# Kernel tuning notes

Measured on AMD Instinct MI355X. Metric: run time of the kernel, lower is better.

## Reference

```python
import jax, jax.numpy as jnp
import numpy as np

SEGMENT_LENGTHS = [1024, 2048, 4096]
DILATION_RATES = [1, 2, 4]


def setup_inputs() -> dict:
    key = jax.random.key(0)
    kq, kk, kv = jax.random.split(key, 3)
    shape = (2, 4096, 12, 64)  # [batch, seq_len, num_heads, head_dim]
    return {
        "query": jax.random.normal(kq, shape, dtype=jnp.float32),
        "key": jax.random.normal(kk, shape, dtype=jnp.float32),
        "value": jax.random.normal(kv, shape, dtype=jnp.float32),
        "is_causal": 0,
    }


def _group_attention(q, k, v, g, r, offset, is_causal):
    """Dilated segment attention for one head group.

    q/k/v: [b, n, hg, d] (head slice for this group).
    Segments of length g; within each segment attend only at positions
    offset, offset+r, ... (m = g // r tokens). Output scattered back to
    those positions; other positions are zero (LongNet semantics).
    """
    b, n, h, d = q.shape
    s = n // g  # number of segments
    m = g // r  # dilated tokens per segment
    idx = offset + r * jnp.arange(m)
    qs = q.reshape(b, s, g, h, d)[:, :, idx]  # [b, s, m, h, d]
    ks = k.reshape(b, s, g, h, d)[:, :, idx]
    vs = v.reshape(b, s, g, h, d)[:, :, idx]
    scale = 1.0 / jnp.sqrt(jnp.asarray(d, dtype=q.dtype))
    scores = jnp.einsum("bsqhd,bskhd->bshqk", qs, ks) * scale  # [b, s, h, m, m]
    if is_causal:
        mask = jnp.tril(jnp.ones((m, m), dtype=bool))
        scores = jnp.where(mask, scores, jnp.finfo(scores.dtype).min)
    probs = jax.nn.softmax(scores, axis=-1)
    o = jnp.einsum("bshqk,bskhd->bsqhd", probs, vs)  # [b, s, m, h, d]
    out = jnp.zeros((b, s, g, h, d), dtype=q.dtype).at[:, :, idx].set(o)
    return out.reshape(b, n, h, d)


def reference(query, key, value, is_causal):
    # dist not initialized -> sequence-parallel split/gather are identity;
    # forward reduces to ImprovedDilatedAttention on full tensors.
    b, n, h, d = query.shape
    ngroups = len(SEGMENT_LENGTHS)
    hpg = h // ngroups  # heads per group (disjoint head slices)
    causal = bool(is_causal)
    outs = []
    for i, (g, r) in enumerate(zip(SEGMENT_LENGTHS, DILATION_RATES)):
        offset = i % r
        hmin, hmax = i * hpg, (i + 1) * hpg
        outs.append(
            _group_attention(
                query[:, :, hmin:hmax],
                key[:, :, hmin:hmax],
                value[:, :, hmin:hmax],
                g, r, offset, causal,
            )
        )
    return jnp.concatenate(outs, axis=2)  # [b, n, h, d]
```

## Files before the change

kernel.cpp:

```cpp
#include <hip/hip_runtime.h>
#include <hip/hip_bf16.h>

typedef __attribute__((ext_vector_type(8))) short short8;
typedef __attribute__((ext_vector_type(4))) float f32x4;

#define NTILE 16

static __device__ __forceinline__ unsigned pk2(float x, float y) {
  __hip_bfloat162 h = __float22bfloat162_rn(make_float2(x, y));
  unsigned u; __builtin_memcpy(&u, &h, 4); return u;
}

static __device__ __forceinline__ short8 cvt8(float4 a, float4 b) {
  union { unsigned u[4]; short8 s; } r;
  r.u[0] = pk2(a.x, a.y); r.u[1] = pk2(a.z, a.w);
  r.u[2] = pk2(b.x, b.y); r.u[3] = pk2(b.z, b.w);
  return r.s;
}

static __device__ __forceinline__ void gll16(const void* g, void* l) {
  __builtin_amdgcn_global_load_lds(
      (__attribute__((address_space(1))) void*)const_cast<void*>(g),
      (__attribute__((address_space(3))) void*)(l), 16, 0, 0);
}

struct InstInfo { long base0; int stride; };
static __device__ __forceinline__ InstInfo decode_inst(int inst) {
  const int gi    = (inst < 32) ? 0 : ((inst < 48) ? 1 : 2);
  const int local = inst - ((gi == 0) ? 0 : ((gi == 1) ? 32 : 48));
  const int segs  = 4 >> gi;
  const int g     = 1024 << gi;
  const int offs  = gi;
  const int h     = local & 3;
  const int rem   = local >> 2;
  const int seg   = rem & (segs - 1);
  const int b     = rem >> (2 - gi);
  const int hh    = gi * 4 + h;
  InstInfo r;
  r.base0  = ((long)(b * 4096 + seg * g + offs) * 12 + hh) * 64;
  r.stride = (1 << gi) * 768;
  return r;
}

__global__ __launch_bounds__(256)
void pack_kv(const float* __restrict__ Kg, const float* __restrict__ Vg,
             unsigned short* __restrict__ Ks, unsigned short* __restrict__ Vts,
             float* __restrict__ Og)
{
  __shared__ float vtmp[64][65];
  const int tid   = threadIdx.x;
  const int lid   = blockIdx.x;
  const int inst  = lid % 56;
  const int chunk = lid / 56;
  const int gi    = (inst < 32) ? 0 : ((inst < 48) ? 1 : 2);
  InstInfo I = decode_inst(inst);

  {
    const int tok = tid >> 2, part = tid & 3;
    const long ro = I.base0 + (long)(chunk * 64 + tok) * I.stride + part * 16;
    const float4 k0 = *(const float4*)(Kg + ro);
    const float4 k1 = *(const float4*)(Kg + ro + 4);
    const float4 k2 = *(const float4*)(Kg + ro + 8);
    const float4 k3 = *(const float4*)(Kg + ro + 12);
    uint4 ka, kb;
    ka.x = pk2(k0.x,k0.y); ka.y = pk2(k0.z,k0.w); ka.z = pk2(k1.x,k1.y); ka.w = pk2(k1.z,k1.w);
    kb.x = pk2(k2.x,k2.y); kb.y = pk2(k2.z,k2.w); kb.z = pk2(k3.x,k3.y); kb.w = pk2(k3.z,k3.w);
    unsigned short* kd = Ks + ((long)inst*1024 + chunk*64 + tok)*64;
    const int c0 = (2*part)     ^ (tok & 7);
    const int c1 = (2*part + 1) ^ (tok & 7);
    *(uint4*)(kd + c0*8) = ka;
    *(uint4*)(kd + c1*8) = kb;

    const float4 w0 = *(const float4*)(Vg + ro);
    const float4 w1 = *(const float4*)(Vg + ro + 4);
    const float4 w2 = *(const float4*)(Vg + ro + 8);
    const float4 w3 = *(const float4*)(Vg + ro + 12);
    float* c = &vtmp[part*16][0] + tok;
    c[0*65]=w0.x;  c[1*65]=w0.y;  c[2*65]=w0.z;  c[3*65]=w0.w;
    c[4*65]=w1.x;  c[5*65]=w1.y;  c[6*65]=w1.z;  c[7*65]=w1.w;
    c[8*65]=w2.x;  c[9*65]=w2.y;  c[10*65]=w2.z; c[11*65]=w2.w;
    c[12*65]=w3.x; c[13*65]=w3.y; c[14*65]=w3.z; c[15*65]=w3.w;
  }
  __syncthreads();
  {
    const int d = tid >> 2, kp = tid & 3;
    float v[16];
#pragma unroll
    for (int i = 0; i < 16; ++i) v[i] = vtmp[d][kp*16 + i];
    unsigned short* vd = Vts + ((long)inst*64 + d)*1024 + chunk*64;
#pragma unroll
    for (int s = 0; s < 2; ++s) {
      const int pos = (kp*2 + s) ^ (d & 7);
      uint4 w;
      w.x = pk2(v[8*s+0], v[8*s+1]); w.y = pk2(v[8*s+2], v[8*s+3]);
      w.z = pk2(v[8*s+4], v[8*s+5]); w.w = pk2(v[8*s+6], v[8*s+7]);
      *(uint4*)(vd + pos*8) = w;
    }
  }

  const float4 z4 = make_float4(0.f, 0.f, 0.f, 0.f);
  if (gi == 1) {
    for (int i = tid; i < 64*16; i += 256) {
      const int t = i >> 4, pp = i & 15;
      float* op = Og + I.base0 + (long)(chunk*128 + 2*t + 0 - 1) * 768 + pp*4;
      *(float4*)op = z4;
    }
  } else if (gi == 2) {
    for (int i = tid; i < 192*16; i += 256) {
      const int row_i = i >> 4, pp = i & 15;
      const int t = row_i / 3, ddi = row_i - 3*t;
      const int dd = ddi + (ddi >= 2 ? 1 : 0);
      float* op = Og + I.base0 + (long)(chunk*256 + 4*t + dd - 2) * 768 + pp*4;
      *(float4*)op = z4;
    }
  }
}

__global__ __launch_bounds__(256, 4)
void dilated_attn2(const float* __restrict__ Qg,
                   const unsigned short* __restrict__ Ks,
                   const unsigned short* __restrict__ Vts,
                   const int* __restrict__ causal_flag,
                   float* __restrict__ Og)
{
  __shared__ __align__(16) unsigned short K_lds[2][64][64];
  __shared__ __align__(16) unsigned short V_lds[2][64][64];
  __shared__ __align__(16) unsigned short P_lds[4][16][64];

  const int tid  = threadIdx.x;
  const int wave = tid >> 6;
  const int lane = tid & 63;
  const int l15  = lane & 15;
  const int l4   = lane >> 4;
  const int sw   = l15 & 7;

  const int lid  = blockIdx.x;
  const int inst = lid % 56;
  const int qt   = lid / 56;
  InstInfo I = decode_inst(inst);
  const int causal = *causal_flag;

  const float qscale = 0.125f * 1.44269504088896340736f;
  short8 b_q[2][2];
  int qrowf[2];
#pragma unroll
  for (int qf = 0; qf < 2; ++qf) {
    qrowf[qf] = qt*128 + wave*32 + qf*16 + l15;
    const float* qp = Qg + I.base0 + (long)qrowf[qf] * I.stride + l4 * 8;
#pragma unroll
    for (int ks = 0; ks < 2; ++ks) {
      float4 v0 = *(const float4*)(qp + ks*32);
      float4 v1 = *(const float4*)(qp + ks*32 + 4);
      v0.x *= qscale; v0.y *= qscale; v0.z *= qscale; v0.w *= qscale;
      v1.x *= qscale; v1.y *= qscale; v1.z *= qscale; v1.w *= qscale;
      b_q[qf][ks] = cvt8(v0, v1);
    }
  }

  short8 ones8;
  {
    union { unsigned u[4]; short8 s; } r;
    r.u[0] = r.u[1] = r.u[2] = r.u[3] = 0x3F803F80u;
    ones8 = r.s;
  }

  const unsigned short* KsI  = Ks  + (long)inst * (1024*64);
  const unsigned short* VtsI = Vts + (long)inst * (64*1024);
  const int vrow = lane >> 3;
  const int vcol = (lane & 7) * 8;

  f32x4 Oacc[2][4];
  f32x4 accl[2];
#pragma unroll
  for (int qf = 0; qf < 2; ++qf) {
    accl[qf] = (f32x4){0.f,0.f,0.f,0.f};
#pragma unroll
    for (int n = 0; n < 4; ++n) Oacc[qf][n] = (f32x4){0.f,0.f,0.f,0.f};
  }

#define STAGE2(BUF, KT) do {                                                      \
    const long tko = (long)(KT) * 4096;                                           \
    gll16(KsI  + tko + (long)(wave*8     + vrow)*64 + vcol, &K_lds[BUF][wave*8][0]);     \
    gll16(KsI  + tko + (long)((wave+4)*8 + vrow)*64 + vcol, &K_lds[BUF][(wave+4)*8][0]); \
    const long vko = (long)(KT) * 64;                                             \
    gll16(VtsI + (long)(wave*8     + vrow)*1024 + vko + vcol, &V_lds[BUF][wave*8][0]);     \
    gll16(VtsI + (long)((wave+4)*8 + vrow)*1024 + vko + vcol, &V_lds[BUF][(wave+4)*8][0]); \
  } while (0)

  STAGE2(0, 0);
  __syncthreads();

  for (int kt = 0; kt < NTILE; ++kt) {
    const int cur = kt & 1;
    if (kt + 1 < NTILE) STAGE2(cur ^ 1, kt + 1);

    f32x4 S[2][4];
#pragma unroll
    for (int n = 0; n < 4; ++n) {
      short8 kA = *(const short8*)&K_lds[cur][n*16 + l15][((l4 ^ sw) & 7) * 8];
      short8 kB = *(const short8*)&K_lds[cur][n*16 + l15][(((4 + l4) ^ sw) & 7) * 8];
      __builtin_amdgcn_s_setprio(1);
      f32x4 a0 = (f32x4){0.f,0.f,0.f,0.f};
      a0 = __builtin_amdgcn_mfma_f32_16x16x32_bf16(kA, b_q[0][0], a0, 0,0,0);
      a0 = __builtin_amdgcn_mfma_f32_16x16x32_bf16(kB, b_q[0][1], a0, 0,0,0);
      S[0][n] = a0;
      f32x4 a1 = (f32x4){0.f,0.f,0.f,0.f};
      a1 = __builtin_amdgcn_mfma_f32_16x16x32_bf16(kA, b_q[1][0], a1, 0,0,0);
      a1 = __builtin_amdgcn_mfma_f32_16x16x32_bf16(kB, b_q[1][1], a1, 0,0,0);
      S[1][n] = a1;
      __builtin_amdgcn_s_setprio(0);
    }

    if (causal) {
#pragma unroll
      for (int qf = 0; qf < 2; ++qf)
#pragma unroll
        for (int n = 0; n < 4; ++n)
#pragma unroll
          for (int j = 0; j < 4; ++j) {
            int ktok = kt*64 + n*16 + l4*4 + j;
            if (ktok > qrowf[qf]) S[qf][n][j] = -INFINITY;
          }
    }

    short8 ap[2][2];
#pragma unroll
    for (int qf = 0; qf < 2; ++qf) {
      unsigned up[4][2];
#pragma unroll
      for (int n = 0; n < 4; ++n)
#pragma unroll
        for (int s = 0; s < 2; ++s) {
          float p0 = __builtin_amdgcn_exp2f(S[qf][n][2*s]);
          float p1 = __builtin_amdgcn_exp2f(S[qf][n][2*s+1]);
          up[n][s] = pk2(p0, p1);
        }
#pragma unroll
      for (int n = 0; n < 4; ++n) {
        const int colblk = (2*n + (l4 >> 1)) ^ sw;
        *(uint2*)&P_lds[wave][l15][colblk*8 + (l4 & 1)*4] = make_uint2(up[n][0], up[n][1]);
      }
      ap[qf][0] = *(const short8*)&P_lds[wave][l15][(l4 ^ sw)*8];
      ap[qf][1] = *(const short8*)&P_lds[wave][l15][((4 + l4) ^ sw)*8];
      accl[qf] = __builtin_amdgcn_mfma_f32_16x16x32_bf16(ap[qf][0], ones8, accl[qf], 0,0,0);
      accl[qf] = __builtin_amdgcn_mfma_f32_16x16x32_bf16(ap[qf][1], ones8, accl[qf], 0,0,0);
    }

#pragma unroll
    for (int n = 0; n < 4; ++n) {
      short8 bv0 = *(const short8*)&V_lds[cur][n*16 + l15][((l4 ^ sw) & 7)*8];
      short8 bv1 = *(const short8*)&V_lds[cur][n*16 + l15][(((4 + l4) ^ sw) & 7)*8];
      __builtin_amdgcn_s_setprio(1);
      Oacc[0][n] = __builtin_amdgcn_mfma_f32_16x16x32_bf16(ap[0][0], bv0, Oacc[0][n], 0,0,0);
      Oacc[0][n] = __builtin_amdgcn_mfma_f32_16x16x32_bf16(ap[0][1], bv1, Oacc[0][n], 0,0,0);
      Oacc[1][n] = __builtin_amdgcn_mfma_f32_16x16x32_bf16(ap[1][0], bv0, Oacc[1][n], 0,0,0);
      Oacc[1][n] = __builtin_amdgcn_mfma_f32_16x16x32_bf16(ap[1][1], bv1, Oacc[1][n], 0,0,0);
      __builtin_amdgcn_s_setprio(0);
    }

    __syncthreads();
  }

  float* ob = Og + I.base0;
#pragma unroll
  for (int qf = 0; qf < 2; ++qf)
#pragma unroll
    for (int j = 0; j < 4; ++j) {
      const float inv = 1.f / accl[qf][j];
      const int qrow = qt*128 + wave*32 + qf*16 + l4*4 + j;
      float* op = ob + (long)qrow * I.stride;
#pragma unroll
      for (int n = 0; n < 4; ++n)
        op[n*16 + l15] = Oacc[qf][n][j] * inv;
    }
}

#define LDP 72
__global__ __launch_bounds__(512, 4)
void dilated_attn_fb(const float* __restrict__ Qg,
                     const float* __restrict__ Kg,
                     const float* __restrict__ Vg,
                     const int* __restrict__ causal_flag,
                     float* __restrict__ Og)
{
  __shared__ __align__(16) unsigned short K_lds[2][64][LDP];
  __shared__ __align__(16) unsigned short Vt_lds[2][64][LDP];
  __shared__ __align__(16) unsigned short P_lds[8][16][LDP];

  const int tid  = threadIdx.x;
  const int wave = tid >> 6;
  const int lane = tid & 63;
  const int l15  = lane & 15;
  const int l4   = lane >> 4;
  const int qt   = blockIdx.x;
  InstInfo I = decode_inst(blockIdx.y);
  const int causal = *causal_flag;

  const float qscale = 0.125f * 1.44269504088896340736f;
  short8 b_q[2];
  {
    const int qrow = qt * 128 + wave * 16 + l15;
    const float* qp = Qg + I.base0 + (long)qrow * I.stride + l4 * 8;
#pragma unroll
    for (int ks = 0; ks < 2; ++ks) {
      float4 v0 = *(const float4*)(qp + ks * 32);
      float4 v1 = *(const float4*)(qp + ks * 32 + 4);
      v0.x *= qscale; v0.y *= qscale; v0.z *= qscale; v0.w *= qscale;
      v1.x *= qscale; v1.y *= qscale; v1.z *= qscale; v1.w *= qscale;
      b_q[ks] = cvt8(v0, v1);
    }
  }
  float m_run = -INFINITY, l_run = 0.f;
  f32x4 Oacc[4];
#pragma unroll
  for (int n = 0; n < 4; ++n) Oacc[n] = (f32x4){0.f,0.f,0.f,0.f};
  const int tt  = tid >> 3;
  const int cb8 = tid & 7;
  const float* kbase = Kg + I.base0 + cb8 * 8;
  const float* vbase = Vg + I.base0 + cb8 * 8;
#define STAGE_FB(BUF, A0, A1, W0, W1) do {                                     \
    *(short8*)&K_lds[BUF][tt][cb8 * 8] = cvt8(A0, A1);                         \
    unsigned p01 = pk2(W0.x, W0.y), p23 = pk2(W0.z, W0.w);                     \
    unsigned p45 = pk2(W1.x, W1.y), p67 = pk2(W1.z, W1.w);                     \
    const int col = (((tt >> 3) ^ cb8) << 3) | (tt & 7);                       \
    Vt_lds[BUF][cb8*8+0][col] = (unsigned short)(p01 & 0xffff);                \
    Vt_lds[BUF][cb8*8+1][col] = (unsigned short)(p01 >> 16);                   \
    Vt_lds[BUF][cb8*8+2][col] = (unsigned short)(p23 & 0xffff);                \
    Vt_lds[BUF][cb8*8+3][col] = (unsigned short)(p23 >> 16);                   \
    Vt_lds[BUF][cb8*8+4][col] = (unsigned short)(p45 & 0xffff);                \
    Vt_lds[BUF][cb8*8+5][col] = (unsigned short)(p45 >> 16);                   \
    Vt_lds[BUF][cb8*8+6][col] = (unsigned short)(p67 & 0xffff);                \
    Vt_lds[BUF][cb8*8+7][col] = (unsigned short)(p67 >> 16);                   \
  } while (0)
  {
    const long ro = (long)tt * I.stride;
    float4 k0 = *(const float4*)(kbase + ro);
    float4 k1 = *(const float4*)(kbase + ro + 4);
    float4 w0 = *(const float4*)(vbase + ro);
    float4 w1 = *(const float4*)(vbase + ro + 4);
    STAGE_FB(0, k0, k1, w0, w1);
  }
  __syncthreads();
  const int qrow_me = qt * 128 + wave * 16 + l15;
  for (int kt = 0; kt < NTILE; ++kt) {
    const int bsel = kt & 1;
    float4 nk0, nk1, nw0, nw1;
    const bool have_next = (kt + 1 < NTILE);
    if (have_next) {
      const long ro = (long)((kt + 1) * 64 + tt) * I.stride;
      nk0 = *(const float4*)(kbase + ro);
      nk1 = *(const float4*)(kbase + ro + 4);
      nw0 = *(const float4*)(vbase + ro);
      nw1 = *(const float4*)(vbase + ro + 4);
    }
    f32x4 S[4];
#pragma unroll
    for (int n = 0; n < 4; ++n) {
      short8 ak0 = *(const short8*)&K_lds[bsel][n*16 + l15][l4*8];
      short8 ak1 = *(const short8*)&K_lds[bsel][n*16 + l15][32 + l4*8];
      f32x4 acc = (f32x4){0.f,0.f,0.f,0.f};
      acc = __builtin_amdgcn_mfma_f32_16x16x32_bf16(ak0, b_q[0], acc, 0,0,0);
      acc = __builtin_amdgcn_mfma_f32_16x16x32_bf16(ak1, b_q[1], acc, 0,0,0);
      S[n] = acc;
    }
    if (causal) {
#pragma unroll
      for (int n = 0; n < 4; ++n)
#pragma unroll
        for (int j = 0; j < 4; ++j) {
          int ktok = kt*64 + n*16 + l4*4 + j;
          if (ktok > qrow_me) S[n][j] = -INFINITY;
        }
    }
    float pmax = S[0][0];
#pragma unroll
    for (int n = 0; n < 4; ++n)
#pragma unroll
      for (int j = 0; j < 4; ++j) pmax = fmaxf(pmax, S[n][j]);
    pmax = fmaxf(pmax, __shfl_xor(pmax, 16));
    pmax = fmaxf(pmax, __shfl_xor(pmax, 32));
    if (!__all(pmax - m_run <= 8.f)) {
      float mn = fmaxf(m_run, pmax);
      float corr = exp2f(m_run - mn);
      m_run = mn; l_run *= corr;
      float cq[4];
#pragma unroll
      for (int j = 0; j < 4; ++j) cq[j] = __shfl(corr, l4*4 + j, 16);
#pragma unroll
      for (int n = 0; n < 4; ++n)
#pragma unroll
        for (int j = 0; j < 4; ++j) Oacc[n][j] *= cq[j];
    }
    float psum = 0.f; unsigned up[4][2];
#pragma unroll
    for (int n = 0; n < 4; ++n)
#pragma unroll
      for (int s = 0; s < 2; ++s) {
        float p0 = exp2f(S[n][2*s]   - m_run);
        float p1 = exp2f(S[n][2*s+1] - m_run);
        psum += p0 + p1; up[n][s] = pk2(p0, p1);
      }
    l_run += psum;
#pragma unroll
    for (int n = 0; n < 4; ++n)
      *(uint2*)&P_lds[wave][l15][n*16 + l4*4] = make_uint2(up[n][0], up[n][1]);
    {
      short8 ap0 = *(const short8*)&P_lds[wave][l15][l4*8];
      short8 ap1 = *(const short8*)&P_lds[wave][l15][32 + l4*8];
#pragma unroll
      for (int n = 0; n < 4; ++n) {
        const int dsw = (2*n + (l15 >> 3)) & 7;
        short8 bv0 = *(const short8*)&Vt_lds[bsel][n*16 + l15][((l4 ^ dsw) & 7)*8];
        short8 bv1 = *(const short8*)&Vt_lds[bsel][n*16 + l15][(((4 + l4) ^ dsw) & 7)*8];
        Oacc[n] = __builtin_amdgcn_mfma_f32_16x16x32_bf16(ap0, bv0, Oacc[n], 0,0,0);
        Oacc[n] = __builtin_amdgcn_mfma_f32_16x16x32_bf16(ap1, bv1, Oacc[n], 0,0,0);
      }
    }
    if (have_next) STAGE_FB(bsel ^ 1, nk0, nk1, nw0, nw1);
    __syncthreads();
  }
  l_run += __shfl_xor(l_run, 16);
  l_run += __shfl_xor(l_run, 32);
  float lq[4];
#pragma unroll
  for (int j = 0; j < 4; ++j) lq[j] = __shfl(l_run, l4*4 + j, 16);
  float* ob = Og + I.base0;
#pragma unroll
  for (int j = 0; j < 4; ++j) {
    const float inv = 1.f / lq[j];
    const int qrow = qt*128 + wave*16 + l4*4 + j;
    float* op = ob + (long)qrow * I.stride;
#pragma unroll
    for (int n = 0; n < 4; ++n)
      op[n*16 + l15] = Oacc[n][j] * inv;
  }
}

extern "C" void kernel_launch(void* const* d_in, const int* in_sizes, int n_in,
                              void* d_out, int out_size, void* d_ws, size_t ws_size,
                              hipStream_t stream) {
  const float* Q = (const float*)d_in[0];
  const float* K = (const float*)d_in[1];
  const float* V = (const float*)d_in[2];
  const int* causal = (const int*)d_in[3];
  float* out = (float*)d_out;

  const size_t per = 56ull * 1024 * 64;
  const size_t need_pack = 2 * per * sizeof(unsigned short);

  if (ws_size >= need_pack) {
    unsigned short* Ks  = (unsigned short*)d_ws;
    unsigned short* Vts = Ks + per;
    pack_kv<<<896, 256, 0, stream>>>(K, V, Ks, Vts, out);
    dilated_attn2<<<448, 256, 0, stream>>>(Q, Ks, Vts, causal, out);
  } else {
    (void)hipMemsetAsync(d_out, 0, (size_t)out_size * sizeof(float), stream);
    dilated_attn_fb<<<dim3(8, 56), 512, 0, stream>>>(Q, K, V, causal, out);
  }
}
```

Before: 40.90 us.

## Feed softmax probabilities directly from registers via 16x16x16 MFMA, dropping P LDS round-trip

When the 16x16x16 bf16 MFMA builtin is available, the probability tile stays in registers: the S accumulator layout already matches the A-operand layout of the K=16 MFMA, so P no longer goes through shared memory. This removes the per-iteration P_lds stores and reloads and frees that LDS. In exchange it issues twice as many MFMAs, each with half the K depth (lower throughput per instruction on CDNA3/4), and V reads become 8-byte loads instead of 16-byte ones. The setprio hints are also dropped in the fallback path.

```diff
diff --git a/kernel.cpp b/kernel.cpp
--- a/kernel.cpp
+++ b/kernel.cpp
@@ -2,9 +2,16 @@
 #include <hip/hip_bf16.h>
 
 typedef __attribute__((ext_vector_type(8))) short short8;
+typedef __attribute__((ext_vector_type(4))) short short4v;
 typedef __attribute__((ext_vector_type(4))) float f32x4;
 
 #define NTILE 16
+
+#if defined(__has_builtin)
+#if __has_builtin(__builtin_amdgcn_mfma_f32_16x16x16bf16_1k)
+#define HAVE_MFMA16 1
+#endif
+#endif
 
 static __device__ __forceinline__ unsigned pk2(float x, float y) {
   __hip_bfloat162 h = __float22bfloat162_rn(make_float2(x, y));
@@ -125,7 +132,9 @@
 {
   __shared__ __align__(16) unsigned short K_lds[2][64][64];
   __shared__ __align__(16) unsigned short V_lds[2][64][64];
+#if !HAVE_MFMA16
   __shared__ __align__(16) unsigned short P_lds[4][16][64];
+#endif
 
   const int tid  = threadIdx.x;
   const int wave = tid >> 6;
@@ -157,12 +166,21 @@
     }
   }
 
+#if HAVE_MFMA16
+  short4v ones4;
+  {
+    union { unsigned u[2]; short4v s; } r;
+    r.u[0] = r.u[1] = 0x3F803F80u;
+    ones4 = r.s;
+  }
+#else
   short8 ones8;
   {
     union { unsigned u[4]; short8 s; } r;
     r.u[0] = r.u[1] = r.u[2] = r.u[3] = 0x3F803F80u;
     ones8 = r.s;
   }
+#endif
 
   const unsigned short* KsI  = Ks  + (long)inst * (1024*64);
   const unsigned short* VtsI = Vts + (long)inst * (64*1024);
@@ -223,6 +241,36 @@
           }
     }
 
+#if HAVE_MFMA16
+    short4v pa[2][4];
+#pragma unroll
+    for (int qf = 0; qf < 2; ++qf)
+#pragma unroll
+      for (int n = 0; n < 4; ++n) {
+        float p0 = __builtin_amdgcn_exp2f(S[qf][n][0]);
+        float p1 = __builtin_amdgcn_exp2f(S[qf][n][1]);
+        float p2 = __builtin_amdgcn_exp2f(S[qf][n][2]);
+        float p3 = __builtin_amdgcn_exp2f(S[qf][n][3]);
+        union { unsigned u[2]; short4v s; } w;
+        w.u[0] = pk2(p0, p1); w.u[1] = pk2(p2, p3);
+        pa[qf][n] = w.s;
+        accl[qf] = __builtin_amdgcn_mfma_f32_16x16x16bf16_1k(pa[qf][n], ones4, accl[qf], 0,0,0);
+      }
+
+#pragma unroll
+    for (int n = 0; n < 4; ++n) {
+      const unsigned short* vrp = &V_lds[cur][n*16 + l15][0];
+      __builtin_amdgcn_s_setprio(1);
+#pragma unroll
+      for (int kb = 0; kb < 4; ++kb) {
+        const int p = ((2*kb + (l4 >> 1)) ^ sw) & 7;
+        short4v bv = *(const short4v*)(vrp + p*8 + (l4 & 1)*4);
+        Oacc[0][n] = __builtin_amdgcn_mfma_f32_16x16x16bf16_1k(pa[0][kb], bv, Oacc[0][n], 0,0,0);
+        Oacc[1][n] = __builtin_amdgcn_mfma_f32_16x16x16bf16_1k(pa[1][kb], bv, Oacc[1][n], 0,0,0);
+      }
+      __builtin_amdgcn_s_setprio(0);
+    }
+#else
     short8 ap[2][2];
 #pragma unroll
     for (int qf = 0; qf < 2; ++qf) {
@@ -245,18 +293,16 @@
       accl[qf] = __builtin_amdgcn_mfma_f32_16x16x32_bf16(ap[qf][0], ones8, accl[qf], 0,0,0);
       accl[qf] = __builtin_amdgcn_mfma_f32_16x16x32_bf16(ap[qf][1], ones8, accl[qf], 0,0,0);
     }
-
 #pragma unroll
     for (int n = 0; n < 4; ++n) {
       short8 bv0 = *(const short8*)&V_lds[cur][n*16 + l15][((l4 ^ sw) & 7)*8];
       short8 bv1 = *(const short8*)&V_lds[cur][n*16 + l15][(((4 + l4) ^ sw) & 7)*8];
-      __builtin_amdgcn_s_setprio(1);
       Oacc[0][n] = __builtin_amdgcn_mfma_f32_16x16x32_bf16(ap[0][0], bv0, Oacc[0][n], 0,0,0);
       Oacc[0][n] = __builtin_amdgcn_mfma_f32_16x16x32_bf16(ap[0][1], bv1, Oacc[0][n], 0,0,0);
       Oacc[1][n] = __builtin_amdgcn_mfma_f32_16x16x32_bf16(ap[1][0], bv0, Oacc[1][n], 0,0,0);
       Oacc[1][n] = __builtin_amdgcn_mfma_f32_16x16x32_bf16(ap[1][1], bv1, Oacc[1][n], 0,0,0);
-      __builtin_amdgcn_s_setprio(0);
-    }
+    }
+#endif
 
     __syncthreads();
   }
```

Result: slower. 41.81 us (+2.2%).
